# Kernel tuning notes

Measured on AMD Instinct MI355X. Metric: run time of the kernel, lower is better.

The kernel has to match this reference:

```python
import jax, jax.numpy as jnp
import numpy as np

N = 50000      # nodes
E = 800000     # edges (before self loops)
FE = 256       # expression features
FC = 128       # CNV features
H = 128        # hidden_channels
NC = 8         # num_classes
C = 512        # number of central nodes


def setup_inputs() -> dict:
    key = jax.random.key(0)
    ks = jax.random.split(key, 24)

    def lin(k, fi, fo):
        k1, k2 = jax.random.split(k)
        s = 1.0 / np.sqrt(fi)
        W = jax.random.uniform(k1, (fi, fo), jnp.float32, -s, s)
        b = jax.random.uniform(k2, (fo,), jnp.float32, -s, s)
        return W, b

    x = jax.random.normal(ks[0], (N, FE), jnp.float32)
    c = jax.random.normal(ks[1], (N, FC), jnp.float32)
    edge_index = jax.random.randint(ks[2], (2, E), 0, N, jnp.int32)
    central_idx = jax.random.randint(ks[3], (C,), 0, N, jnp.int32)

    W1e, b1e = lin(ks[4], FE, H)
    W2e, b2e = lin(ks[5], H, H)
    W1c, b1c = lin(ks[6], FC, H)
    W2c, b2c = lin(ks[7], H, H)
    Wm, bm = lin(ks[8], 2 * H, NC)
    Wp1, bp1 = lin(ks[9], NC, H)
    Wp2, bp2 = lin(ks[10], H, NC)

    return dict(
        x=x, c=c, edge_index=edge_index, central_idx=central_idx,
        me_x=jax.random.normal(ks[11], (FE,), jnp.float32),
        me_c=jax.random.normal(ks[12], (FC,), jnp.float32),
        W1e=W1e, b1e=b1e, eps1e=jnp.float32(0.0),
        W2e=W2e, b2e=b2e, eps2e=jnp.float32(0.0),
        W1c=W1c, b1c=b1c, eps1c=jnp.float32(0.0),
        W2c=W2c, b2c=b2c, eps2c=jnp.float32(0.0),
        Wm=Wm, bm=bm, Wp1=Wp1, bp1=bp1, Wp2=Wp2, bp2=bp2,
    )


def _gin_conv(h, src, dst, eps, W, b):
    # GINConv with nn = Linear: lin((1+eps)*x + sum_{j in N(i)} x_j)
    agg = jax.ops.segment_sum(h[src], dst, num_segments=N)  # scatter-add of messages
    return ((1.0 + eps) * h + agg) @ W + b


def reference(x, c, edge_index, central_idx, me_x, me_c,
              W1e, b1e, eps1e, W2e, b2e, eps2e,
              W1c, b1c, eps1c, W2c, b2c, eps2c,
              Wm, bm, Wp1, bp1, Wp2, bp2):
    lrelu = lambda v: jax.nn.leaky_relu(v, 0.2)

    # add self loops
    loops = jnp.arange(N, dtype=edge_index.dtype)
    src = jnp.concatenate([edge_index[0], loops])
    dst = jnp.concatenate([edge_index[1], loops])

    # replace exact-zero entries with learned missing embeddings (broadcast per row)
    x = jnp.where(x == 0, me_x[None, :], x)
    c = jnp.where(c == 0, me_c[None, :], c)

    x_exp = lrelu(_gin_conv(x, src, dst, eps1e, W1e, b1e))
    x_exp = lrelu(_gin_conv(x_exp, src, dst, eps2e, W2e, b2e))

    x_cnv = lrelu(_gin_conv(c, src, dst, eps1c, W1c, b1c))
    x_cnv = lrelu(_gin_conv(x_cnv, src, dst, eps2c, W2c, b2c))

    h = jnp.concatenate([x_exp, x_cnv], axis=1)          # [N, 2H]
    out = lrelu(h @ Wm + bm)                             # [N, NC]

    central = out[central_idx]                           # [C, NC]
    logits = jax.nn.relu(central @ Wp1 + bp1) @ Wp2 + bp2
    return out, logits
```

## Files before the change

kernel.cpp:

```cpp
#include <hip/hip_runtime.h>

typedef unsigned short u16;
typedef __attribute__((ext_vector_type(8))) short short8;
typedef __attribute__((ext_vector_type(4))) float floatx4;

__device__ __forceinline__ float b2f(unsigned int ubits) {
  union { unsigned int i; float f; } cv; cv.i = ubits << 16; return cv.f;
}
__device__ __forceinline__ float hi2f(unsigned int u) {
  union { unsigned int i; float f; } cv; cv.i = u & 0xffff0000u; return cv.f;
}
__device__ __forceinline__ float lo2f(unsigned int u) {
  union { unsigned int i; float f; } cv; cv.i = u << 16; return cv.f;
}
__device__ __forceinline__ u16 f2b(float f) {
  unsigned int u = __builtin_bit_cast(unsigned int, f);
  u += 0x7fffu + ((u >> 16) & 1u);
  return (u16)(u >> 16);
}
__device__ __forceinline__ float lrelu(float v) { return v > 0.f ? v : 0.2f * v; }
__device__ __forceinline__ float rdf(bool isbf, const void* p, int idx) {
  return isbf ? b2f((unsigned int)((const u16*)p)[idx]) : ((const float*)p)[idx];
}

__global__ void detect_kernel(const u16* __restrict__ probe, int* __restrict__ flag) {
  int lane = threadIdx.x;
  int cnt = 0;
  for (int i = lane; i < 256; i += 64) {
    unsigned int u = probe[i];
    unsigned int e = (u >> 7) & 0xFFu;
    if ((u & 0x7fffu) == 0 || (e >= 60 && e <= 191)) cnt++;
  }
#pragma unroll
  for (int off = 32; off; off >>= 1) cnt += __shfl_down(cnt, off, 64);
  if (lane == 0) *flag = (cnt >= 240) ? 1 : 0;
}

__global__ __launch_bounds__(256) void hist_kernel(const int* __restrict__ dst, int E,
                                                   int* __restrict__ deg) {
  int i = blockIdx.x * 256 + threadIdx.x;
  if (i < E) atomicAdd(deg + dst[i], 1);
}

#define SCB 1024

__global__ __launch_bounds__(256) void scan_phaseA(const int* __restrict__ deg,
                                                   int* __restrict__ bsum, int n) {
  int i0 = blockIdx.x * SCB + threadIdx.x * 4;
  int s = 0;
  if (i0 + 3 < n) {
    int4 v = *(const int4*)(deg + i0);
    s = v.x + v.y + v.z + v.w;
  } else {
    for (int j = 0; j < 4; j++) if (i0 + j < n) s += deg[i0 + j];
  }
#pragma unroll
  for (int off = 32; off; off >>= 1) s += __shfl_down(s, off, 64);
  __shared__ int ws4[4];
  int lane = threadIdx.x & 63, wid = threadIdx.x >> 6;
  if (lane == 0) ws4[wid] = s;
  __syncthreads();
  if (threadIdx.x == 0) bsum[blockIdx.x] = ws4[0] + ws4[1] + ws4[2] + ws4[3];
}

__global__ void scan_phaseB(const int* __restrict__ bsum, int* __restrict__ boff,
                            int PB, int* __restrict__ rowptr, int n) {
  int lane = threadIdx.x;
  int v = (lane < PB) ? bsum[lane] : 0;
  int incl = v;
#pragma unroll
  for (int off = 1; off < 64; off <<= 1) {
    int t = __shfl_up(incl, off, 64);
    if (lane >= off) incl += t;
  }
  if (lane < PB) boff[lane] = incl - v;
  if (lane == 63) rowptr[n] = incl;
}

__global__ __launch_bounds__(256) void scan_phaseC(const int* __restrict__ deg,
                                                   const int* __restrict__ boff,
                                                   int* __restrict__ rowptr,
                                                   int* __restrict__ cursor, int n) {
  int i0 = blockIdx.x * SCB + threadIdx.x * 4;
  int v0 = 0, v1 = 0, v2 = 0, v3 = 0;
  if (i0 + 3 < n) {
    int4 v = *(const int4*)(deg + i0);
    v0 = v.x; v1 = v.y; v2 = v.z; v3 = v.w;
  } else {
    if (i0 < n) v0 = deg[i0];
    if (i0 + 1 < n) v1 = deg[i0 + 1];
    if (i0 + 2 < n) v2 = deg[i0 + 2];
    if (i0 + 3 < n) v3 = deg[i0 + 3];
  }
  int local = v0 + v1 + v2 + v3;
  int lane = threadIdx.x & 63, wid = threadIdx.x >> 6;
  int incl = local;
#pragma unroll
  for (int off = 1; off < 64; off <<= 1) {
    int t = __shfl_up(incl, off, 64);
    if (lane >= off) incl += t;
  }
  __shared__ int ws4[4];
  if (lane == 63) ws4[wid] = incl;
  __syncthreads();
  int woff = 0;
  for (int w = 0; w < wid; w++) woff += ws4[w];
  int run = boff[blockIdx.x] + woff + incl - local;
  if (i0 < n)     { rowptr[i0] = run;     cursor[i0] = run; }     run += v0;
  if (i0 + 1 < n) { rowptr[i0 + 1] = run; cursor[i0 + 1] = run; } run += v1;
  if (i0 + 2 < n) { rowptr[i0 + 2] = run; cursor[i0 + 2] = run; } run += v2;
  if (i0 + 3 < n) { rowptr[i0 + 3] = run; cursor[i0 + 3] = run; }
}

__global__ __launch_bounds__(256) void fill_kernel(const int* __restrict__ src,
                                                   const int* __restrict__ dst, int E,
                                                   int* __restrict__ cursor,
                                                   int* __restrict__ colarr) {
  int i = blockIdx.x * 256 + threadIdx.x;
  if (i < E) {
    int p = atomicAdd(cursor + dst[i], 1);
    colarr[p] = src[i];
  }
}

struct TWDesc {
  const void* W[5];
  int K[5];
  int Nc[5];
  int base[6];
};

__global__ __launch_bounds__(256) void transpose_all(TWDesc d, u16* __restrict__ out,
                                                     const int* __restrict__ flagp) {
  bool isbf = (*flagp != 0);
  int idx = blockIdx.x * 256 + threadIdx.x;
  if (idx >= d.base[5]) return;
  int s = 0;
  while (idx >= d.base[s + 1]) s++;
  int local = idx - d.base[s];
  int K = d.K[s], Nc = d.Nc[s];
  int nn = local / K;
  int k = local - nn * K;
  out[idx] = (nn < Nc) ? f2b(rdf(isbf, d.W[s], k * Nc + nn)) : (u16)0;
}

template <int NSUB, bool RAW_A, bool HAS_ME, bool HAS_EPI, bool OUT_F32>
__global__ __launch_bounds__(256) void mfma_gemm(
    const void* __restrict__ Av, int lda,
    const void* __restrict__ me,
    const u16* __restrict__ Bt, int K, int M,
    void* __restrict__ C, int ldc, int colofs, int ncols,
    const void* __restrict__ bias, const int* __restrict__ flagp) {
  bool isbf = (*flagp != 0);
  int wid = threadIdx.x >> 6;
  int lane = threadIdx.x & 63;
  int l15 = lane & 15;
  int q = lane >> 4;
  int row0 = blockIdx.x * 64 + wid * 16;

  floatx4 acc[NSUB];
#pragma unroll
  for (int n = 0; n < NSUB; n++) acc[n] = (floatx4){0.f, 0.f, 0.f, 0.f};

  int r = row0 + l15;
  if (r >= M) r = M - 1;

  for (int k0 = 0; k0 < K; k0 += 32) {
    short8 a;
    if (!RAW_A || isbf) {
      const u16* A = (const u16*)Av;
      a = *(const short8*)(A + (long)r * lda + k0 + q * 8);
      if (HAS_ME) {
#pragma unroll
        for (int j = 0; j < 8; j++) {
          if (((u16)a[j] & 0x7fffu) == 0)
            a[j] = (short)f2b(rdf(isbf, me, k0 + q * 8 + j));
        }
      }
    } else {
      const float* A = (const float*)Av;
      const uint4* p = (const uint4*)(A + (long)r * lda + k0 + q * 8);
      uint4 w0 = p[0];
      uint4 w1 = p[1];
      unsigned int ww[8] = {w0.x, w0.y, w0.z, w0.w, w1.x, w1.y, w1.z, w1.w};
#pragma unroll
      for (int j = 0; j < 8; j++) {
        if (HAS_ME && (ww[j] & 0x7fffffffu) == 0)
          a[j] = (short)f2b(((const float*)me)[k0 + q * 8 + j]);
        else
          a[j] = (short)f2b(__builtin_bit_cast(float, ww[j]));
      }
    }
#pragma unroll
    for (int n = 0; n < NSUB; n++) {
      short8 b = *(const short8*)(Bt + (n * 16 + l15) * K + k0 + q * 8);
      acc[n] = __builtin_amdgcn_mfma_f32_16x16x32_bf16(a, b, acc[n], 0, 0, 0);
    }
  }

#pragma unroll
  for (int n = 0; n < NSUB; n++)
#pragma unroll
    for (int rr = 0; rr < 4; rr++) {
      int row = row0 + q * 4 + rr;
      int col = n * 16 + l15;
      if (row < M && col < ncols) {
        float v = acc[n][rr];
        if (HAS_EPI) {
          v += rdf(isbf, bias, col);
          v = lrelu(v);
        }
        if (OUT_F32)
          ((float*)C)[(long)row * ldc + colofs + col] = v;
        else
          ((u16*)C)[(long)row * ldc + colofs + col] = f2b(v);
      }
    }
}

__global__ __launch_bounds__(256) void agg_kernel(
    const u16* __restrict__ t, const int* __restrict__ rowptr, const int* __restrict__ colarr,
    const void* __restrict__ epsE, const void* __restrict__ epsC,
    const void* __restrict__ bE, const void* __restrict__ bC,
    u16* __restrict__ u, int N, const int* __restrict__ flagp) {
  int node = blockIdx.x * 8 + (threadIdx.x >> 5);
  if (node >= N) return;
  bool isbf = (*flagp != 0);
  int lane = threadIdx.x & 31;
  int f0 = lane << 3;
  const u16* tb = t + f0;
  float a0 = 0.f, a1 = 0.f, a2 = 0.f, a3 = 0.f, a4 = 0.f, a5 = 0.f, a6 = 0.f, a7 = 0.f;
  int e = rowptr[node], e1 = rowptr[node + 1];
#define ACC8(p)                                                   \
  a0 += lo2f(p.x); a1 += hi2f(p.x); a2 += lo2f(p.y); a3 += hi2f(p.y); \
  a4 += lo2f(p.z); a5 += hi2f(p.z); a6 += lo2f(p.w); a7 += hi2f(p.w);
  for (; e + 4 <= e1; e += 4) {
    int c0 = colarr[e], c1 = colarr[e + 1], c2 = colarr[e + 2], c3 = colarr[e + 3];
    uint4 p0 = *(const uint4*)(tb + ((long)c0 << 8));
    uint4 p1 = *(const uint4*)(tb + ((long)c1 << 8));
    uint4 p2 = *(const uint4*)(tb + ((long)c2 << 8));
    uint4 p3 = *(const uint4*)(tb + ((long)c3 << 8));
    ACC8(p0) ACC8(p1) ACC8(p2) ACC8(p3)
  }
  for (; e < e1; e++) {
    int c = colarr[e];
    uint4 p = *(const uint4*)(tb + ((long)c << 8));
    ACC8(p)
  }
#undef ACC8
  uint4 ps = *(const uint4*)(tb + ((long)node << 8));
  bool isE = (f0 < 128);
  float eps2 = 2.0f + rdf(isbf, isE ? epsE : epsC, 0);
  const void* bp = isE ? bE : bC;
  int bi = isE ? f0 : (f0 - 128);
  a0 = lrelu(a0 + eps2 * lo2f(ps.x) + rdf(isbf, bp, bi + 0));
  a1 = lrelu(a1 + eps2 * hi2f(ps.x) + rdf(isbf, bp, bi + 1));
  a2 = lrelu(a2 + eps2 * lo2f(ps.y) + rdf(isbf, bp, bi + 2));
  a3 = lrelu(a3 + eps2 * hi2f(ps.y) + rdf(isbf, bp, bi + 3));
  a4 = lrelu(a4 + eps2 * lo2f(ps.z) + rdf(isbf, bp, bi + 4));
  a5 = lrelu(a5 + eps2 * hi2f(ps.z) + rdf(isbf, bp, bi + 5));
  a6 = lrelu(a6 + eps2 * lo2f(ps.w) + rdf(isbf, bp, bi + 6));
  a7 = lrelu(a7 + eps2 * hi2f(ps.w) + rdf(isbf, bp, bi + 7));
  uint4 o;
  o.x = ((unsigned int)f2b(a1) << 16) | f2b(a0);
  o.y = ((unsigned int)f2b(a3) << 16) | f2b(a2);
  o.z = ((unsigned int)f2b(a5) << 16) | f2b(a4);
  o.w = ((unsigned int)f2b(a7) << 16) | f2b(a6);
  *(uint4*)(u + ((long)node << 8) + f0) = o;
}

__global__ __launch_bounds__(128) void mlp_kernel(
    const float* __restrict__ outbuf, const int* __restrict__ central,
    const void* __restrict__ Wp1, const void* __restrict__ bp1,
    const void* __restrict__ Wp2, const void* __restrict__ bp2,
    float* __restrict__ logits, const int* __restrict__ flagp) {
  __shared__ float h1[128];
  __shared__ float o[8];
  bool isbf = (*flagp != 0);
  int b = blockIdx.x, tid = threadIdx.x;
  int node = central[b];
  if (tid < 8) o[tid] = outbuf[node * 8 + tid];
  __syncthreads();
  float s = rdf(isbf, bp1, tid);
#pragma unroll
  for (int k = 0; k < 8; k++) s += o[k] * rdf(isbf, Wp1, k * 128 + tid);
  h1[tid] = fmaxf(s, 0.f);
  __syncthreads();
  if (tid < 8) {
    float s2 = rdf(isbf, bp2, tid);
    for (int k = 0; k < 128; k++) s2 += h1[k] * rdf(isbf, Wp2, k * 8 + tid);
    logits[b * 8 + tid] = s2;
  }
}

extern "C" void kernel_launch(void* const* d_in, const int* in_sizes, int n_in,
                              void* d_out, int out_size, void* d_ws, size_t ws_size,
                              hipStream_t stream) {
  const void* x    = d_in[0];
  const void* c    = d_in[1];
  const int* eidx  = (const int*)d_in[2];
  const int* cidx  = (const int*)d_in[3];
  const void* me_x = d_in[4];
  const void* me_c = d_in[5];
  const void* W1e  = d_in[6];
  const void* b1e  = d_in[7];
  const void* e1e  = d_in[8];
  const void* W2e  = d_in[9];
  const void* b2e  = d_in[10];
  const void* e2e  = d_in[11];
  const void* W1c  = d_in[12];
  const void* b1c  = d_in[13];
  const void* e1c  = d_in[14];
  const void* W2c  = d_in[15];
  const void* b2c  = d_in[16];
  const void* e2c  = d_in[17];
  const void* Wm   = d_in[18];
  const void* bm   = d_in[19];
  const void* Wp1  = d_in[20];
  const void* bp1  = d_in[21];
  const void* Wp2  = d_in[22];
  const void* bp2  = d_in[23];

  const int N = in_sizes[0] / 256;
  const int E = in_sizes[2] / 2;
  const int Cn = in_sizes[3];
  const int* src = eidx;
  const int* dst = eidx + E;

  char* ws = (char*)d_ws;
  int* deg    = (int*)(ws + 0);
  int* rowptr = (int*)(ws + 200192);
  int* cursor = (int*)(ws + 400384);
  int* colarr = (int*)(ws + 600576);
  u16* tbuf   = (u16*)(ws + 3800576);
  u16* ubuf   = (u16*)(ws + 29400576);
  u16* wt_all = (u16*)(ws + 55000576);
  int* flag   = (int*)(ws + 55172608);
  int* bsum   = (int*)(ws + 55172864);
  int* boff   = (int*)(ws + 55173120);

  u16* w1e_t = wt_all + 0;
  u16* w1c_t = wt_all + 32768;
  u16* w2e_t = wt_all + 49152;
  u16* w2c_t = wt_all + 65536;
  u16* wm_t  = wt_all + 81920;

  detect_kernel<<<1, 64, 0, stream>>>((const u16*)x, flag);

  hipMemsetAsync(deg, 0, (size_t)N * 4, stream);
  hist_kernel<<<(E + 255) / 256, 256, 0, stream>>>(dst, E, deg);
  int PB = (N + SCB - 1) / SCB;
  scan_phaseA<<<PB, 256, 0, stream>>>(deg, bsum, N);
  scan_phaseB<<<1, 64, 0, stream>>>(bsum, boff, PB, rowptr, N);
  scan_phaseC<<<PB, 256, 0, stream>>>(deg, boff, rowptr, cursor, N);
  fill_kernel<<<(E + 255) / 256, 256, 0, stream>>>(src, dst, E, cursor, colarr);

  TWDesc td;
  td.W[0] = W1e; td.K[0] = 256; td.Nc[0] = 128;
  td.W[1] = W1c; td.K[1] = 128; td.Nc[1] = 128;
  td.W[2] = W2e; td.K[2] = 128; td.Nc[2] = 128;
  td.W[3] = W2c; td.K[3] = 128; td.Nc[3] = 128;
  td.W[4] = Wm;  td.K[4] = 256; td.Nc[4] = 8;
  td.base[0] = 0; td.base[1] = 32768; td.base[2] = 49152;
  td.base[3] = 65536; td.base[4] = 81920; td.base[5] = 86016;
  transpose_all<<<(86016 + 255) / 256, 256, 0, stream>>>(td, wt_all, flag);

  int gb = (N + 63) / 64;
  mfma_gemm<8, true, true, false, false><<<gb, 256, 0, stream>>>(
      x, 256, me_x, w1e_t, 256, N, tbuf, 256, 0, 128, nullptr, flag);
  mfma_gemm<8, true, true, false, false><<<gb, 256, 0, stream>>>(
      c, 128, me_c, w1c_t, 128, N, tbuf, 256, 128, 128, nullptr, flag);
  agg_kernel<<<(N + 7) / 8, 256, 0, stream>>>(tbuf, rowptr, colarr,
      e1e, e1c, b1e, b1c, ubuf, N, flag);

  mfma_gemm<8, false, false, false, false><<<gb, 256, 0, stream>>>(
      ubuf, 256, nullptr, w2e_t, 128, N, tbuf, 256, 0, 128, nullptr, flag);
  mfma_gemm<8, false, false, false, false><<<gb, 256, 0, stream>>>(
      (const u16*)ubuf + 128, 256, nullptr, w2c_t, 128, N, tbuf, 256, 128, 128, nullptr, flag);
  agg_kernel<<<(N + 7) / 8, 256, 0, stream>>>(tbuf, rowptr, colarr,
      e2e, e2c, b2e, b2c, ubuf, N, flag);

  mfma_gemm<1, false, false, true, true><<<gb, 256, 0, stream>>>(
      ubuf, 256, nullptr, wm_t, 256, N, d_out, 8, 0, 8, bm, flag);

  mlp_kernel<<<Cn, 128, 0, stream>>>((const float*)d_out, cidx,
      Wp1, bp1, Wp2, bp2, (float*)d_out + (size_t)N * 8, flag);
}
```

Baseline: 488.7 us.

## Fuse GIN layer GEMMs, fold head projection into final aggregation, merge init kernels

Merges the detect kernel with zeroing of the degree array. Combines the paired expression/CNV GEMMs for each layer into one kernel per layer. Fuses the final Wm projection with bias and leaky ReLU into the second aggregation kernel, using shared-memory weights and wave shuffle reductions, which removes the ubuf round trip and one launch. Aggregation now uses one 64-lane wave per node with 4 features per lane instead of 32 lanes with 8. This trades wider gather vectors for more wave-level parallelism and adds reduction work in the head.

```diff
diff --git a/kernel.cpp b/kernel.cpp
--- a/kernel.cpp
+++ b/kernel.cpp
@@ -23,17 +23,27 @@
   return isbf ? b2f((unsigned int)((const u16*)p)[idx]) : ((const float*)p)[idx];
 }
 
-__global__ void detect_kernel(const u16* __restrict__ probe, int* __restrict__ flag) {
-  int lane = threadIdx.x;
-  int cnt = 0;
-  for (int i = lane; i < 256; i += 64) {
-    unsigned int u = probe[i];
-    unsigned int e = (u >> 7) & 0xFFu;
-    if ((u & 0x7fffu) == 0 || (e >= 60 && e <= 191)) cnt++;
-  }
-#pragma unroll
-  for (int off = 32; off; off >>= 1) cnt += __shfl_down(cnt, off, 64);
-  if (lane == 0) *flag = (cnt >= 240) ? 1 : 0;
+__global__ __launch_bounds__(256) void init_kernel(int* __restrict__ deg, int n,
+                                                   const u16* __restrict__ probe,
+                                                   int* __restrict__ flag) {
+  int i0 = (blockIdx.x * 256 + threadIdx.x) * 4;
+  if (i0 + 3 < n) {
+    *(int4*)(deg + i0) = make_int4(0, 0, 0, 0);
+  } else {
+    for (int j = 0; j < 4; j++) if (i0 + j < n) deg[i0 + j] = 0;
+  }
+  if (blockIdx.x == 0 && threadIdx.x < 64) {
+    int lane = threadIdx.x;
+    int cnt = 0;
+    for (int i = lane; i < 256; i += 64) {
+      unsigned int u = probe[i];
+      unsigned int e = (u >> 7) & 0xFFu;
+      if ((u & 0x7fffu) == 0 || (e >= 60 && e <= 191)) cnt++;
+    }
+#pragma unroll
+    for (int off = 32; off; off >>= 1) cnt += __shfl_down(cnt, off, 64);
+    if (lane == 0) *flag = (cnt >= 240) ? 1 : 0;
+  }
 }
 
 __global__ __launch_bounds__(256) void hist_kernel(const int* __restrict__ dst, int E,
@@ -144,76 +154,114 @@
   out[idx] = (nn < Nc) ? f2b(rdf(isbf, d.W[s], k * Nc + nn)) : (u16)0;
 }
 
-template <int NSUB, bool RAW_A, bool HAS_ME, bool HAS_EPI, bool OUT_F32>
-__global__ __launch_bounds__(256) void mfma_gemm(
-    const void* __restrict__ Av, int lda,
-    const void* __restrict__ me,
-    const u16* __restrict__ Bt, int K, int M,
-    void* __restrict__ C, int ldc, int colofs, int ncols,
-    const void* __restrict__ bias, const int* __restrict__ flagp) {
+__device__ __forceinline__ short8 load_a_me(const void* Av, int lda, const void* me,
+                                            int r, int k0, int q, bool isbf) {
+  short8 a;
+  if (isbf) {
+    a = *(const short8*)((const u16*)Av + (long)r * lda + k0 + q * 8);
+#pragma unroll
+    for (int j = 0; j < 8; j++) {
+      if (((u16)a[j] & 0x7fffu) == 0)
+        a[j] = (short)((const u16*)me)[k0 + q * 8 + j];
+    }
+  } else {
+    const float* A = (const float*)Av;
+    const uint4* p = (const uint4*)(A + (long)r * lda + k0 + q * 8);
+    uint4 w0 = p[0];
+    uint4 w1 = p[1];
+    unsigned int ww[8] = {w0.x, w0.y, w0.z, w0.w, w1.x, w1.y, w1.z, w1.w};
+#pragma unroll
+    for (int j = 0; j < 8; j++) {
+      if ((ww[j] & 0x7fffffffu) == 0)
+        a[j] = (short)f2b(((const float*)me)[k0 + q * 8 + j]);
+      else
+        a[j] = (short)f2b(__builtin_bit_cast(float, ww[j]));
+    }
+  }
+  return a;
+}
+
+__global__ __launch_bounds__(256) void gemm_l1(
+    const void* __restrict__ x, const void* __restrict__ cc,
+    const void* __restrict__ mex, const void* __restrict__ mec,
+    const u16* __restrict__ w1e_t, const u16* __restrict__ w1c_t,
+    int M, u16* __restrict__ tb, const int* __restrict__ flagp) {
   bool isbf = (*flagp != 0);
   int wid = threadIdx.x >> 6;
   int lane = threadIdx.x & 63;
   int l15 = lane & 15;
   int q = lane >> 4;
   int row0 = blockIdx.x * 64 + wid * 16;
-
-  floatx4 acc[NSUB];
-#pragma unroll
-  for (int n = 0; n < NSUB; n++) acc[n] = (floatx4){0.f, 0.f, 0.f, 0.f};
-
   int r = row0 + l15;
   if (r >= M) r = M - 1;
 
-  for (int k0 = 0; k0 < K; k0 += 32) {
-    short8 a;
-    if (!RAW_A || isbf) {
-      const u16* A = (const u16*)Av;
-      a = *(const short8*)(A + (long)r * lda + k0 + q * 8);
-      if (HAS_ME) {
-#pragma unroll
-        for (int j = 0; j < 8; j++) {
-          if (((u16)a[j] & 0x7fffu) == 0)
-            a[j] = (short)f2b(rdf(isbf, me, k0 + q * 8 + j));
-        }
-      }
-    } else {
-      const float* A = (const float*)Av;
-      const uint4* p = (const uint4*)(A + (long)r * lda + k0 + q * 8);
-      uint4 w0 = p[0];
-      uint4 w1 = p[1];
-      unsigned int ww[8] = {w0.x, w0.y, w0.z, w0.w, w1.x, w1.y, w1.z, w1.w};
-#pragma unroll
-      for (int j = 0; j < 8; j++) {
-        if (HAS_ME && (ww[j] & 0x7fffffffu) == 0)
-          a[j] = (short)f2b(((const float*)me)[k0 + q * 8 + j]);
-        else
-          a[j] = (short)f2b(__builtin_bit_cast(float, ww[j]));
-      }
-    }
-#pragma unroll
-    for (int n = 0; n < NSUB; n++) {
-      short8 b = *(const short8*)(Bt + (n * 16 + l15) * K + k0 + q * 8);
-      acc[n] = __builtin_amdgcn_mfma_f32_16x16x32_bf16(a, b, acc[n], 0, 0, 0);
-    }
-  }
-
-#pragma unroll
-  for (int n = 0; n < NSUB; n++)
+  floatx4 acce[8], accc[8];
+#pragma unroll
+  for (int n = 0; n < 8; n++) { acce[n] = (floatx4){0,0,0,0}; accc[n] = (floatx4){0,0,0,0}; }
+
+  for (int k0 = 0; k0 < 256; k0 += 32) {
+    short8 a = load_a_me(x, 256, mex, r, k0, q, isbf);
+#pragma unroll
+    for (int n = 0; n < 8; n++) {
+      short8 b = *(const short8*)(w1e_t + (n * 16 + l15) * 256 + k0 + q * 8);
+      acce[n] = __builtin_amdgcn_mfma_f32_16x16x32_bf16(a, b, acce[n], 0, 0, 0);
+    }
+  }
+  for (int k0 = 0; k0 < 128; k0 += 32) {
+    short8 a = load_a_me(cc, 128, mec, r, k0, q, isbf);
+#pragma unroll
+    for (int n = 0; n < 8; n++) {
+      short8 b = *(const short8*)(w1c_t + (n * 16 + l15) * 128 + k0 + q * 8);
+      accc[n] = __builtin_amdgcn_mfma_f32_16x16x32_bf16(a, b, accc[n], 0, 0, 0);
+    }
+  }
+#pragma unroll
+  for (int n = 0; n < 8; n++)
 #pragma unroll
     for (int rr = 0; rr < 4; rr++) {
       int row = row0 + q * 4 + rr;
-      int col = n * 16 + l15;
-      if (row < M && col < ncols) {
-        float v = acc[n][rr];
-        if (HAS_EPI) {
-          v += rdf(isbf, bias, col);
-          v = lrelu(v);
-        }
-        if (OUT_F32)
-          ((float*)C)[(long)row * ldc + colofs + col] = v;
-        else
-          ((u16*)C)[(long)row * ldc + colofs + col] = f2b(v);
+      if (row < M) {
+        tb[(long)row * 256 + n * 16 + l15] = f2b(acce[n][rr]);
+        tb[(long)row * 256 + 128 + n * 16 + l15] = f2b(accc[n][rr]);
+      }
+    }
+}
+
+__global__ __launch_bounds__(256) void gemm_l2(
+    const u16* __restrict__ u,
+    const u16* __restrict__ w2e_t, const u16* __restrict__ w2c_t,
+    int M, u16* __restrict__ tb) {
+  int wid = threadIdx.x >> 6;
+  int lane = threadIdx.x & 63;
+  int l15 = lane & 15;
+  int q = lane >> 4;
+  int row0 = blockIdx.x * 64 + wid * 16;
+  int r = row0 + l15;
+  if (r >= M) r = M - 1;
+
+  floatx4 acce[8], accc[8];
+#pragma unroll
+  for (int n = 0; n < 8; n++) { acce[n] = (floatx4){0,0,0,0}; accc[n] = (floatx4){0,0,0,0}; }
+
+  for (int k0 = 0; k0 < 128; k0 += 32) {
+    short8 ae = *(const short8*)(u + (long)r * 256 + k0 + q * 8);
+    short8 ac = *(const short8*)(u + (long)r * 256 + 128 + k0 + q * 8);
+#pragma unroll
+    for (int n = 0; n < 8; n++) {
+      short8 be = *(const short8*)(w2e_t + (n * 16 + l15) * 128 + k0 + q * 8);
+      short8 bc = *(const short8*)(w2c_t + (n * 16 + l15) * 128 + k0 + q * 8);
+      acce[n] = __builtin_amdgcn_mfma_f32_16x16x32_bf16(ae, be, acce[n], 0, 0, 0);
+      accc[n] = __builtin_amdgcn_mfma_f32_16x16x32_bf16(ac, bc, accc[n], 0, 0, 0);
+    }
+  }
+#pragma unroll
+  for (int n = 0; n < 8; n++)
+#pragma unroll
+    for (int rr = 0; rr < 4; rr++) {
+      int row = row0 + q * 4 + rr;
+      if (row < M) {
+        tb[(long)row * 256 + n * 16 + l15] = f2b(acce[n][rr]);
+        tb[(long)row * 256 + 128 + n * 16 + l15] = f2b(accc[n][rr]);
       }
     }
 }
@@ -223,33 +271,32 @@
     const void* __restrict__ epsE, const void* __restrict__ epsC,
     const void* __restrict__ bE, const void* __restrict__ bC,
     u16* __restrict__ u, int N, const int* __restrict__ flagp) {
-  int node = blockIdx.x * 8 + (threadIdx.x >> 5);
+  int node = blockIdx.x * 4 + (threadIdx.x >> 6);
   if (node >= N) return;
   bool isbf = (*flagp != 0);
-  int lane = threadIdx.x & 31;
-  int f0 = lane << 3;
+  int lane = threadIdx.x & 63;
+  int f0 = lane << 2;
   const u16* tb = t + f0;
-  float a0 = 0.f, a1 = 0.f, a2 = 0.f, a3 = 0.f, a4 = 0.f, a5 = 0.f, a6 = 0.f, a7 = 0.f;
+  float a0 = 0.f, a1 = 0.f, a2 = 0.f, a3 = 0.f;
   int e = rowptr[node], e1 = rowptr[node + 1];
-#define ACC8(p)                                                   \
-  a0 += lo2f(p.x); a1 += hi2f(p.x); a2 += lo2f(p.y); a3 += hi2f(p.y); \
-  a4 += lo2f(p.z); a5 += hi2f(p.z); a6 += lo2f(p.w); a7 += hi2f(p.w);
   for (; e + 4 <= e1; e += 4) {
     int c0 = colarr[e], c1 = colarr[e + 1], c2 = colarr[e + 2], c3 = colarr[e + 3];
-    uint4 p0 = *(const uint4*)(tb + ((long)c0 << 8));
-    uint4 p1 = *(const uint4*)(tb + ((long)c1 << 8));
-    uint4 p2 = *(const uint4*)(tb + ((long)c2 << 8));
-    uint4 p3 = *(const uint4*)(tb + ((long)c3 << 8));
-    ACC8(p0) ACC8(p1) ACC8(p2) ACC8(p3)
+    uint2 p0 = *(const uint2*)(tb + ((long)c0 << 8));
+    uint2 p1 = *(const uint2*)(tb + ((long)c1 << 8));
+    uint2 p2 = *(const uint2*)(tb + ((long)c2 << 8));
+    uint2 p3 = *(const uint2*)(tb + ((long)c3 << 8));
+    a0 += lo2f(p0.x); a1 += hi2f(p0.x); a2 += lo2f(p0.y); a3 += hi2f(p0.y);
+    a0 += lo2f(p1.x); a1 += hi2f(p1.x); a2 += lo2f(p1.y); a3 += hi2f(p1.y);
+    a0 += lo2f(p2.x); a1 += hi2f(p2.x); a2 += lo2f(p2.y); a3 += hi2f(p2.y);
+    a0 += lo2f(p3.x); a1 += hi2f(p3.x); a2 += lo2f(p3.y); a3 += hi2f(p3.y);
   }
   for (; e < e1; e++) {
     int c = colarr[e];
-    uint4 p = *(const uint4*)(tb + ((long)c << 8));
-    ACC8(p)
-  }
-#undef ACC8
-  uint4 ps = *(const uint4*)(tb + ((long)node << 8));
-  bool isE = (f0 < 128);
+    uint2 p = *(const uint2*)(tb + ((long)c << 8));
+    a0 += lo2f(p.x); a1 += hi2f(p.x); a2 += lo2f(p.y); a3 += hi2f(p.y);
+  }
+  uint2 ps = *(const uint2*)(tb + ((long)node << 8));
+  bool isE = (lane < 32);
   float eps2 = 2.0f + rdf(isbf, isE ? epsE : epsC, 0);
   const void* bp = isE ? bE : bC;
   int bi = isE ? f0 : (f0 - 128);
@@ -257,16 +304,79 @@
   a1 = lrelu(a1 + eps2 * hi2f(ps.x) + rdf(isbf, bp, bi + 1));
   a2 = lrelu(a2 + eps2 * lo2f(ps.y) + rdf(isbf, bp, bi + 2));
   a3 = lrelu(a3 + eps2 * hi2f(ps.y) + rdf(isbf, bp, bi + 3));
-  a4 = lrelu(a4 + eps2 * lo2f(ps.z) + rdf(isbf, bp, bi + 4));
-  a5 = lrelu(a5 + eps2 * hi2f(ps.z) + rdf(isbf, bp, bi + 5));
-  a6 = lrelu(a6 + eps2 * lo2f(ps.w) + rdf(isbf, bp, bi + 6));
-  a7 = lrelu(a7 + eps2 * hi2f(ps.w) + rdf(isbf, bp, bi + 7));
-  uint4 o;
+  uint2 o;
   o.x = ((unsigned int)f2b(a1) << 16) | f2b(a0);
   o.y = ((unsigned int)f2b(a3) << 16) | f2b(a2);
-  o.z = ((unsigned int)f2b(a5) << 16) | f2b(a4);
-  o.w = ((unsigned int)f2b(a7) << 16) | f2b(a6);
-  *(uint4*)(u + ((long)node << 8) + f0) = o;
+  *(uint2*)(u + ((long)node << 8) + f0) = o;
+}
+
+__global__ __launch_bounds__(256) void agg_head(
+    const u16* __restrict__ t, const int* __restrict__ rowptr, const int* __restrict__ colarr,
+    const void* __restrict__ epsE, const void* __restrict__ epsC,
+    const void* __restrict__ bE, const void* __restrict__ bC,
+    const u16* __restrict__ wm_t, const void* __restrict__ bm,
+    float* __restrict__ out, int N, const int* __restrict__ flagp) {
+  __shared__ float wmf[2048];
+  __shared__ float bmf[8];
+  bool isbf = (*flagp != 0);
+  int tid = threadIdx.x;
+  for (int i = tid; i < 2048; i += 256) wmf[i] = b2f((unsigned int)wm_t[i]);
+  if (tid < 8) bmf[tid] = rdf(isbf, bm, tid);
+  __syncthreads();
+
+  int node = blockIdx.x * 4 + (tid >> 6);
+  if (node >= N) return;
+  int lane = tid & 63;
+  int f0 = lane << 2;
+  const u16* tb = t + f0;
+  float a0 = 0.f, a1 = 0.f, a2 = 0.f, a3 = 0.f;
+  int e = rowptr[node], e1 = rowptr[node + 1];
+  for (; e + 4 <= e1; e += 4) {
+    int c0 = colarr[e], c1 = colarr[e + 1], c2 = colarr[e + 2], c3 = colarr[e + 3];
+    uint2 p0 = *(const uint2*)(tb + ((long)c0 << 8));
+    uint2 p1 = *(const uint2*)(tb + ((long)c1 << 8));
+    uint2 p2 = *(const uint2*)(tb + ((long)c2 << 8));
+    uint2 p3 = *(const uint2*)(tb + ((long)c3 << 8));
+    a0 += lo2f(p0.x); a1 += hi2f(p0.x); a2 += lo2f(p0.y); a3 += hi2f(p0.y);
+    a0 += lo2f(p1.x); a1 += hi2f(p1.x); a2 += lo2f(p1.y); a3 += hi2f(p1.y);
+    a0 += lo2f(p2.x); a1 += hi2f(p2.x); a2 += lo2f(p2.y); a3 += hi2f(p2.y);
+    a0 += lo2f(p3.x); a1 += hi2f(p3.x); a2 += lo2f(p3.y); a3 += hi2f(p3.y);
+  }
+  for (; e < e1; e++) {
+    int c = colarr[e];
+    uint2 p = *(const uint2*)(tb + ((long)c << 8));
+    a0 += lo2f(p.x); a1 += hi2f(p.x); a2 += lo2f(p.y); a3 += hi2f(p.y);
+  }
+  uint2 ps = *(const uint2*)(tb + ((long)node << 8));
+  bool isE = (lane < 32);
+  float eps2 = 2.0f + rdf(isbf, isE ? epsE : epsC, 0);
+  const void* bp = isE ? bE : bC;
+  int bi = isE ? f0 : (f0 - 128);
+  a0 = lrelu(a0 + eps2 * lo2f(ps.x) + rdf(isbf, bp, bi + 0));
+  a1 = lrelu(a1 + eps2 * hi2f(ps.x) + rdf(isbf, bp, bi + 1));
+  a2 = lrelu(a2 + eps2 * lo2f(ps.y) + rdf(isbf, bp, bi + 2));
+  a3 = lrelu(a3 + eps2 * hi2f(ps.y) + rdf(isbf, bp, bi + 3));
+
+  float p[8];
+#pragma unroll
+  for (int col = 0; col < 8; col++) {
+    float4 w = *(const float4*)&wmf[col * 256 + f0];
+    p[col] = a0 * w.x + a1 * w.y + a2 * w.z + a3 * w.w;
+  }
+#pragma unroll
+  for (int m = 1; m < 64; m <<= 1) {
+#pragma unroll
+    for (int col = 0; col < 8; col++) p[col] += __shfl_xor(p[col], m, 64);
+  }
+  if (lane == 0) {
+    float4 o0, o1;
+    o0.x = lrelu(p[0] + bmf[0]); o0.y = lrelu(p[1] + bmf[1]);
+    o0.z = lrelu(p[2] + bmf[2]); o0.w = lrelu(p[3] + bmf[3]);
+    o1.x = lrelu(p[4] + bmf[4]); o1.y = lrelu(p[5] + bmf[5]);
+    o1.z = lrelu(p[6] + bmf[6]); o1.w = lrelu(p[7] + bmf[7]);
+    *(float4*)(out + (long)node * 8) = o0;
+    *(float4*)(out + (long)node * 8 + 4) = o1;
+  }
 }
 
 __global__ __launch_bounds__(128) void mlp_kernel(
@@ -345,9 +455,8 @@
   u16* w2c_t = wt_all + 65536;
   u16* wm_t  = wt_all + 81920;
 
-  detect_kernel<<<1, 64, 0, stream>>>((const u16*)x, flag);
-
-  hipMemsetAsync(deg, 0, (size_t)N * 4, stream);
+  init_kernel<<<(N + 1023) / 1024, 256, 0, stream>>>(deg, N, (const u16*)x, flag);
+
   hist_kernel<<<(E + 255) / 256, 256, 0, stream>>>(dst, E, deg);
   int PB = (N + SCB - 1) / SCB;
   scan_phaseA<<<PB, 256, 0, stream>>>(deg, bsum, N);
@@ -366,23 +475,12 @@
   transpose_all<<<(86016 + 255) / 256, 256, 0, stream>>>(td, wt_all, flag);
 
   int gb = (N + 63) / 64;
-  mfma_gemm<8, true, true, false, false><<<gb, 256, 0, stream>>>(
-      x, 256, me_x, w1e_t, 256, N, tbuf, 256, 0, 128, nullptr, flag);
-  mfma_gemm<8, true, true, false, false><<<gb, 256, 0, stream>>>(
-      c, 128, me_c, w1c_t, 128, N, tbuf, 256, 128, 128, nullptr, flag);
-  agg_kernel<<<(N + 7) / 8, 256, 0, stream>>>(tbuf, rowptr, colarr,
+  gemm_l1<<<gb, 256, 0, stream>>>(x, c, me_x, me_c, w1e_t, w1c_t, N, tbuf, flag);
+  agg_kernel<<<(N + 3) / 4, 256, 0, stream>>>(tbuf, rowptr, colarr,
       e1e, e1c, b1e, b1c, ubuf, N, flag);
-
-  mfma_gemm<8, false, false, false, false><<<gb, 256, 0, stream>>>(
-      ubuf, 256, nullptr, w2e_t, 128, N, tbuf, 256, 0, 128, nullptr, flag);
-  mfma_gemm<8, false, false, false, false><<<gb, 256, 0, stream>>>(
-      (const u16*)ubuf + 128, 256, nullptr, w2c_t, 128, N, tbuf, 256, 128, 128, nullptr, flag);
-  agg_kernel<<<(N + 7) / 8, 256, 0, stream>>>(tbuf, rowptr, colarr,
-      e2e, e2c, b2e, b2c, ubuf, N, flag);
-
-  mfma_gemm<1, false, false, true, true><<<gb, 256, 0, stream>>>(
-      ubuf, 256, nullptr, wm_t, 256, N, d_out, 8, 0, 8, bm, flag);
-
+  gemm_l2<<<gb, 256, 0, stream>>>(ubuf, w2e_t, w2c_t, N, tbuf);
+  agg_head<<<(N + 3) / 4, 256, 0, stream>>>(tbuf, rowptr, colarr,
+      e2e, e2c, b2e, b2c, wm_t, bm, (float*)d_out, N, flag);
   mlp_kernel<<<Cn, 128, 0, stream>>>((const float*)d_out, cidx,
       Wp1, bp1, Wp2, bp2, (float*)d_out + (size_t)N * 8, flag);
 }
```

Measured after the change: 464.7 us. 1.05x faster.
